# Kernel optimization log

Hardware: AMD Instinct MI355X
Metric: run time of the kernel (lower is better)

## Reference

```python
import jax, jax.numpy as jnp
import numpy as np

SAMPLE_RATE = 0.1
BINS = int(256 * SAMPLE_RATE)  # 25
KSIZE = 7
EPS = 1e-6


def _pascal_kernel_2d(ksize):
    # kornia get_pascal_kernel_2d(ksize, norm=True): outer product of binomial row, sum=1
    row = np.array([1.0, 6.0, 15.0, 20.0, 15.0, 6.0, 1.0], dtype=np.float32)
    row = row / row.sum()
    k2d = np.outer(row, row)
    return jnp.asarray(k2d, dtype=jnp.float32)


def _blur_pool2d(x, ksize=KSIZE):
    # kornia.filters.blur_pool2d: depthwise conv with pascal kernel, stride 2, zero pad ksize//2
    C = x.shape[1]
    k = jnp.broadcast_to(_pascal_kernel_2d(ksize).astype(x.dtype), (C, 1, ksize, ksize))
    pad = ksize // 2
    return jax.lax.conv_general_dilated(
        x, k, window_strides=(2, 2), padding=((pad, pad), (pad, pad)),
        feature_group_count=C, dimension_numbers=("NCHW", "OIHW", "NCHW"))


def _per_channel_hist(x, bins):
    # torch.histc(v, bins, 0, 1) per (b, c) plane: values outside [0,1] ignored,
    # value == 1 falls in last bin. Fused via one flat scatter-add.
    B, C, H, W = x.shape
    v = x.reshape(B * C, H * W)
    idx = jnp.clip(jnp.floor(v * bins).astype(jnp.int32), 0, bins - 1)
    valid = ((v >= 0.0) & (v <= 1.0)).astype(x.dtype)
    flat_idx = (jnp.arange(B * C, dtype=jnp.int32)[:, None] * bins + idx).reshape(-1)
    hist = jnp.zeros(B * C * bins, dtype=x.dtype).at[flat_idx].add(valid.reshape(-1))
    return hist.reshape(B, C, bins)


def setup_inputs() -> dict:
    key = jax.random.key(0)
    kx, ky = jax.random.split(key)
    B, C, H, W = 32, 3, 512, 512
    x = jax.random.uniform(kx, (B, C, H, W), dtype=jnp.float32)
    y = jax.random.uniform(ky, (B, C, H, W), dtype=jnp.float32)
    return {"x": x, "y": y}


def reference(x, y):
    hw = x.shape[-2] * x.shape[-1]  # original H*W (as in source)
    xb = _blur_pool2d(x)
    yb = _blur_pool2d(y)
    xh = _per_channel_hist(xb, BINS) / hw  # [B, C, BINS]
    yh = _per_channel_hist(yb, BINS) / hw
    # nn.CosineSimilarity(dim=0, eps=1e-6) applied per (b, c) vector pair
    dot = jnp.sum(xh * yh, axis=-1)
    nx = jnp.maximum(jnp.linalg.norm(xh, axis=-1), EPS)
    ny = jnp.maximum(jnp.linalg.norm(yh, axis=-1), EPS)
    cos = dot / (nx * ny)  # [B, C]
    return jnp.mean(cos)
```

## Files before the change

kernel.cpp:

```cpp
#include <hip/hip_runtime.h>

#define BINS 25
#define H 512
#define W 512
#define OH 256
#define OW 256
#define NPLANES 96
#define TOX 32
#define TOY 16
#define NBX 8
#define NBY 16
#define NBLK (NBX*NBY)
#define TROWS 37
#define LDW 72
#define RP 72
#define VP 36
#define NPAIR 35

__global__ __launch_bounds__(256) void blur_hist(
        const float* __restrict__ x, const float* __restrict__ y,
        unsigned int* __restrict__ partial) {
    const int z = blockIdx.z;
    const float* src = (z < NPLANES) ? x + (size_t)z * H * W
                                     : y + (size_t)(z - NPLANES) * H * W;

    __shared__ __align__(16) float raw[TROWS * RP];
    __shared__ float ve[TOY * VP];
    __shared__ float vo[TOY * VP];
    __shared__ unsigned int sh[4 * 32];

    const int tid = threadIdx.x;
    const int base_x = 2 * (blockIdx.x * TOX) - 4;
    const int base_y = 2 * (blockIdx.y * TOY) - 3;

    if (tid < 128) sh[tid] = 0u;

    const bool xfull = (base_x >= 0) && (base_x + LDW <= W);
    for (int v = tid; v < TROWS * (LDW / 4); v += 256) {
        int r  = v / (LDW / 4);
        int c4 = v - r * (LDW / 4);
        int gy = base_y + r;
        int gx = base_x + 4 * c4;
        float4 val = make_float4(0.f, 0.f, 0.f, 0.f);
        if (gy >= 0 && gy < H) {
            if (xfull) {
                val = *(const float4*)(src + (size_t)gy * W + gx);
            } else {
                const size_t rb = (size_t)gy * W;
                if (gx + 0 >= 0 && gx + 0 < W) val.x = src[rb + gx + 0];
                if (gx + 1 >= 0 && gx + 1 < W) val.y = src[rb + gx + 1];
                if (gx + 2 >= 0 && gx + 2 < W) val.z = src[rb + gx + 2];
                if (gx + 3 >= 0 && gx + 3 < W) val.w = src[rb + gx + 3];
            }
        }
        *(float4*)(raw + r * RP + 4 * c4) = val;
    }
    __syncthreads();

    const float w0 = 1.f/64.f, w1 = 6.f/64.f, w2 = 15.f/64.f, w3 = 20.f/64.f;

    for (int v = tid; v < TOY * NPAIR; v += 256) {
        int ly = v / NPAIR;
        int pr = v - ly * NPAIR;
        const float2* p = (const float2*)(raw + 2 * ly * RP + 2 * pr);
        float2 a0 = p[0 * (RP/2)], a1 = p[1 * (RP/2)], a2 = p[2 * (RP/2)],
               a3 = p[3 * (RP/2)], a4 = p[4 * (RP/2)], a5 = p[5 * (RP/2)],
               a6 = p[6 * (RP/2)];
        ve[ly * VP + pr] = w0*(a0.x+a6.x) + w1*(a1.x+a5.x) + w2*(a2.x+a4.x) + w3*a3.x;
        vo[ly * VP + pr] = w0*(a0.y+a6.y) + w1*(a1.y+a5.y) + w2*(a2.y+a4.y) + w3*a3.y;
    }
    __syncthreads();

    const int lx = tid & 31;
    unsigned int* wh = &sh[(tid >> 6) * 32];
    #pragma unroll
    for (int i = 0; i < 2; i++) {
        int ly = (tid >> 5) + 8 * i;
        const float* e = ve + ly * VP + lx;
        const float* o = vo + ly * VP + lx;
        float s = w0*(o[0] + o[3]) + w2*(o[1] + o[2]) + w1*(e[1] + e[3]) + w3*e[2];
        int b = min((int)(s * 25.f), BINS - 1);
        atomicAdd(&wh[b], 1u);
    }
    __syncthreads();

    if (tid < BINS) {
        unsigned int t = sh[tid] + sh[32 + tid] + sh[64 + tid] + sh[96 + tid];
        int blk = blockIdx.y * NBX + blockIdx.x;
        partial[((size_t)z * NBLK + blk) * BINS + tid] = t;
    }
}

__global__ __launch_bounds__(256) void reduce_cos(
        const unsigned int* __restrict__ partial, float* __restrict__ out) {
    __shared__ unsigned int sh[2 * BINS];
    const int p = blockIdx.x;
    const int t = threadIdx.x;
    if (t < 2 * BINS) sh[t] = 0u;
    __syncthreads();
    const unsigned int* xp = partial + (size_t)p * NBLK * BINS;
    const unsigned int* yp = partial + (size_t)(NPLANES + p) * NBLK * BINS;
    for (int f = t; f < NBLK * BINS; f += 256) {
        int b = f % BINS;
        atomicAdd(&sh[b], xp[f]);
        atomicAdd(&sh[BINS + b], yp[f]);
    }
    __syncthreads();
    if (t == 0) {
        const float inv_hw = 1.0f / (float)(H * W);
        float dot = 0.f, nx = 0.f, ny = 0.f;
        for (int i = 0; i < BINS; i++) {
            float a = (float)sh[i] * inv_hw;
            float b = (float)sh[BINS + i] * inv_hw;
            dot += a * b;
            nx  += a * a;
            ny  += b * b;
        }
        nx = fmaxf(sqrtf(nx), 1e-6f);
        ny = fmaxf(sqrtf(ny), 1e-6f);
        atomicAdd(out, (dot / (nx * ny)) * (1.0f / (float)NPLANES));
    }
}

extern "C" void kernel_launch(void* const* d_in, const int* in_sizes, int n_in,
                              void* d_out, int out_size, void* d_ws, size_t ws_size,
                              hipStream_t stream) {
    const float* x = (const float*)d_in[0];
    const float* y = (const float*)d_in[1];
    float* out = (float*)d_out;

    unsigned int* partial = (unsigned int*)d_ws;

    hipMemsetAsync(out, 0, sizeof(float), stream);

    dim3 grd(NBX, NBY, 2 * NPLANES);
    blur_hist<<<grd, 256, 0, stream>>>(x, y, partial);

    reduce_cos<<<NPLANES, 256, 0, stream>>>(partial, out);
}
```

Baseline: 232.2 us.

## Use async global-to-LDS loads for interior tiles and lane-private histograms

```diff
diff --git a/kernel.cpp b/kernel.cpp
--- a/kernel.cpp
+++ b/kernel.cpp
@@ -3,8 +3,6 @@
 #define BINS 25
 #define H 512
 #define W 512
-#define OH 256
-#define OW 256
 #define NPLANES 96
 #define TOX 32
 #define TOY 16
@@ -12,10 +10,17 @@
 #define NBY 16
 #define NBLK (NBX*NBY)
 #define TROWS 37
-#define LDW 72
 #define RP 72
+#define NV4 (TROWS*18)
 #define VP 36
-#define NPAIR 35
+#define NSH 32
+
+__device__ __forceinline__ void async_load16(const float* g, float* lds_wave_base) {
+    __builtin_amdgcn_global_load_lds(
+        (const __attribute__((address_space(1))) void*)g,
+        (__attribute__((address_space(3))) void*)lds_wave_base,
+        16, 0, 0);
+}
 
 __global__ __launch_bounds__(256) void blur_hist(
         const float* __restrict__ x, const float* __restrict__ y,
@@ -27,52 +32,68 @@
     __shared__ __align__(16) float raw[TROWS * RP];
     __shared__ float ve[TOY * VP];
     __shared__ float vo[TOY * VP];
-    __shared__ unsigned int sh[4 * 32];
+    __shared__ unsigned int sh[NSH * BINS];
 
     const int tid = threadIdx.x;
     const int base_x = 2 * (blockIdx.x * TOX) - 4;
     const int base_y = 2 * (blockIdx.y * TOY) - 3;
 
-    if (tid < 128) sh[tid] = 0u;
+    for (int i = tid; i < NSH * BINS; i += 256) sh[i] = 0u;
 
-    const bool xfull = (base_x >= 0) && (base_x + LDW <= W);
-    for (int v = tid; v < TROWS * (LDW / 4); v += 256) {
-        int r  = v / (LDW / 4);
-        int c4 = v - r * (LDW / 4);
-        int gy = base_y + r;
-        int gx = base_x + 4 * c4;
-        float4 val = make_float4(0.f, 0.f, 0.f, 0.f);
-        if (gy >= 0 && gy < H) {
-            if (xfull) {
-                val = *(const float4*)(src + (size_t)gy * W + gx);
-            } else {
-                const size_t rb = (size_t)gy * W;
-                if (gx + 0 >= 0 && gx + 0 < W) val.x = src[rb + gx + 0];
-                if (gx + 1 >= 0 && gx + 1 < W) val.y = src[rb + gx + 1];
-                if (gx + 2 >= 0 && gx + 2 < W) val.z = src[rb + gx + 2];
-                if (gx + 3 >= 0 && gx + 3 < W) val.w = src[rb + gx + 3];
+    const bool interior = (base_x >= 0) && (base_x + RP <= W) &&
+                          (base_y >= 0) && (base_y + TROWS <= H);
+    if (interior) {
+        #pragma unroll
+        for (int k = 0; k < 3; k++) {
+            int v = 256 * k + tid;
+            if (v < NV4) {
+                int r = v / 18;
+                int c = v - r * 18;
+                const float* g = src + (size_t)(base_y + r) * W + base_x + 4 * c;
+                float* dst = raw + (size_t)(256 * k + (tid & ~63)) * 4;
+                async_load16(g, dst);
             }
         }
-        *(float4*)(raw + r * RP + 4 * c4) = val;
+    } else {
+        const bool xfull = (base_x >= 0) && (base_x + RP <= W);
+        for (int v = tid; v < NV4; v += 256) {
+            int r  = v / 18;
+            int c4 = v - r * 18;
+            int gy = base_y + r;
+            int gx = base_x + 4 * c4;
+            float4 val = make_float4(0.f, 0.f, 0.f, 0.f);
+            if (gy >= 0 && gy < H) {
+                if (xfull) {
+                    val = *(const float4*)(src + (size_t)gy * W + gx);
+                } else {
+                    const size_t rb = (size_t)gy * W;
+                    if (gx + 0 >= 0 && gx + 0 < W) val.x = src[rb + gx + 0];
+                    if (gx + 1 >= 0 && gx + 1 < W) val.y = src[rb + gx + 1];
+                    if (gx + 2 >= 0 && gx + 2 < W) val.z = src[rb + gx + 2];
+                    if (gx + 3 >= 0 && gx + 3 < W) val.w = src[rb + gx + 3];
+                }
+            }
+            *(float4*)(raw + r * RP + 4 * c4) = val;
+        }
     }
     __syncthreads();
 
     const float w0 = 1.f/64.f, w1 = 6.f/64.f, w2 = 15.f/64.f, w3 = 20.f/64.f;
 
-    for (int v = tid; v < TOY * NPAIR; v += 256) {
-        int ly = v / NPAIR;
-        int pr = v - ly * NPAIR;
-        const float2* p = (const float2*)(raw + 2 * ly * RP + 2 * pr);
-        float2 a0 = p[0 * (RP/2)], a1 = p[1 * (RP/2)], a2 = p[2 * (RP/2)],
-               a3 = p[3 * (RP/2)], a4 = p[4 * (RP/2)], a5 = p[5 * (RP/2)],
-               a6 = p[6 * (RP/2)];
-        ve[ly * VP + pr] = w0*(a0.x+a6.x) + w1*(a1.x+a5.x) + w2*(a2.x+a4.x) + w3*a3.x;
-        vo[ly * VP + pr] = w0*(a0.y+a6.y) + w1*(a1.y+a5.y) + w2*(a2.y+a4.y) + w3*a3.y;
+    for (int v = tid; v < TOY * 70; v += 256) {
+        int ly = v / 70;
+        int t  = v - ly * 70;
+        const float* p = raw + (2 * ly) * RP + t;
+        float s = w0 * (p[0] + p[6 * RP]) + w1 * (p[1 * RP] + p[5 * RP])
+                + w2 * (p[2 * RP] + p[4 * RP]) + w3 * p[3 * RP];
+        int pr = t >> 1;
+        if (t & 1) vo[ly * VP + pr] = s;
+        else       ve[ly * VP + pr] = s;
     }
     __syncthreads();
 
     const int lx = tid & 31;
-    unsigned int* wh = &sh[(tid >> 6) * 32];
+    unsigned int* wh = sh + (tid & 31) * BINS;
     #pragma unroll
     for (int i = 0; i < 2; i++) {
         int ly = (tid >> 5) + 8 * i;
@@ -85,9 +106,11 @@
     __syncthreads();
 
     if (tid < BINS) {
-        unsigned int t = sh[tid] + sh[32 + tid] + sh[64 + tid] + sh[96 + tid];
+        unsigned int s = 0;
+        #pragma unroll
+        for (int g = 0; g < NSH; g++) s += sh[g * BINS + tid];
         int blk = blockIdx.y * NBX + blockIdx.x;
-        partial[((size_t)z * NBLK + blk) * BINS + tid] = t;
+        partial[((size_t)z * NBLK + blk) * BINS + tid] = s;
     }
 }
 
```

Measured after the change: 231.6 us. About the same (-0.3%).

## Replace shared-memory tiled blur with register sliding-window column strips

Applied to the files above, without the earlier changes.

```diff
diff --git a/kernel.cpp b/kernel.cpp
--- a/kernel.cpp
+++ b/kernel.cpp
@@ -3,118 +3,114 @@
 #define BINS 25
 #define H 512
 #define W 512
-#define OH 256
-#define OW 256
 #define NPLANES 96
-#define TOX 32
-#define TOY 16
-#define NBX 8
-#define NBY 16
-#define NBLK (NBX*NBY)
-#define TROWS 37
-#define LDW 72
-#define RP 72
-#define VP 36
-#define NPAIR 35
+#define NSH 32
 
 __global__ __launch_bounds__(256) void blur_hist(
         const float* __restrict__ x, const float* __restrict__ y,
         unsigned int* __restrict__ partial) {
-    const int z = blockIdx.z;
+    const int b = blockIdx.x;
+    const int z = b >> 2;
     const float* src = (z < NPLANES) ? x + (size_t)z * H * W
                                      : y + (size_t)(z - NPLANES) * H * W;
 
-    __shared__ __align__(16) float raw[TROWS * RP];
-    __shared__ float ve[TOY * VP];
-    __shared__ float vo[TOY * VP];
-    __shared__ unsigned int sh[4 * 32];
+    __shared__ unsigned int sh[NSH * BINS];
+    const int tid = threadIdx.x;
+    if (tid < (NSH * BINS / 4))
+        *(float4*)((float*)sh + 4 * tid) = make_float4(0.f, 0.f, 0.f, 0.f);
+    __syncthreads();
 
-    const int tid = threadIdx.x;
-    const int base_x = 2 * (blockIdx.x * TOX) - 4;
-    const int base_y = 2 * (blockIdx.y * TOY) - 3;
-
-    if (tid < 128) sh[tid] = 0u;
-
-    const bool xfull = (base_x >= 0) && (base_x + LDW <= W);
-    for (int v = tid; v < TROWS * (LDW / 4); v += 256) {
-        int r  = v / (LDW / 4);
-        int c4 = v - r * (LDW / 4);
-        int gy = base_y + r;
-        int gx = base_x + 4 * c4;
-        float4 val = make_float4(0.f, 0.f, 0.f, 0.f);
-        if (gy >= 0 && gy < H) {
-            if (xfull) {
-                val = *(const float4*)(src + (size_t)gy * W + gx);
-            } else {
-                const size_t rb = (size_t)gy * W;
-                if (gx + 0 >= 0 && gx + 0 < W) val.x = src[rb + gx + 0];
-                if (gx + 1 >= 0 && gx + 1 < W) val.y = src[rb + gx + 1];
-                if (gx + 2 >= 0 && gx + 2 < W) val.z = src[rb + gx + 2];
-                if (gx + 3 >= 0 && gx + 3 < W) val.w = src[rb + gx + 3];
-            }
-        }
-        *(float4*)(raw + r * RP + 4 * c4) = val;
-    }
-    __syncthreads();
+    const int i = tid & 63;
+    const int s = (b & 3) * 4 + (tid >> 6);
+    const int c0 = 8 * i - 4;
+    const int o0 = (i == 0)  ? 0   : c0;
+    const int o3 = (i == 63) ? 508 : c0 + 12;
+    const float m0 = (i == 0)  ? 0.f : 1.f;
+    const float m3 = (i == 63) ? 0.f : 1.f;
 
     const float w0 = 1.f/64.f, w1 = 6.f/64.f, w2 = 15.f/64.f, w3 = 20.f/64.f;
 
-    for (int v = tid; v < TOY * NPAIR; v += 256) {
-        int ly = v / NPAIR;
-        int pr = v - ly * NPAIR;
-        const float2* p = (const float2*)(raw + 2 * ly * RP + 2 * pr);
-        float2 a0 = p[0 * (RP/2)], a1 = p[1 * (RP/2)], a2 = p[2 * (RP/2)],
-               a3 = p[3 * (RP/2)], a4 = p[4 * (RP/2)], a5 = p[5 * (RP/2)],
-               a6 = p[6 * (RP/2)];
-        ve[ly * VP + pr] = w0*(a0.x+a6.x) + w1*(a1.x+a5.x) + w2*(a2.x+a4.x) + w3*a3.x;
-        vo[ly * VP + pr] = w0*(a0.y+a6.y) + w1*(a1.y+a5.y) + w2*(a2.y+a4.y) + w3*a3.y;
+    auto load_row = [&](int gy) -> float4 {
+        float4 h = make_float4(0.f, 0.f, 0.f, 0.f);
+        if ((unsigned)gy < (unsigned)H) {
+            const float* rp = src + (size_t)gy * W;
+            float4 Q0 = *(const float4*)(rp + o0);
+            float4 Q1 = *(const float4*)(rp + c0 + 4);
+            float4 Q2 = *(const float4*)(rp + c0 + 8);
+            float4 Q3 = *(const float4*)(rp + o3);
+            float r1 = Q0.y * m0, r2 = Q0.z * m0, r3 = Q0.w * m0;
+            float r4 = Q1.x, r5 = Q1.y, r6 = Q1.z, r7 = Q1.w;
+            float r8 = Q2.x, r9 = Q2.y, r10 = Q2.z, r11 = Q2.w;
+            float r12 = Q3.x * m3, r13 = Q3.y * m3;
+            h.x = w0*(r1 + r7)  + w1*(r2 + r6)  + w2*(r3 + r5)  + w3*r4;
+            h.y = w0*(r3 + r9)  + w1*(r4 + r8)  + w2*(r5 + r7)  + w3*r6;
+            h.z = w0*(r5 + r11) + w1*(r6 + r10) + w2*(r7 + r9)  + w3*r8;
+            h.w = w0*(r7 + r13) + w1*(r8 + r12) + w2*(r9 + r11) + w3*r10;
+        }
+        return h;
+    };
+
+    unsigned int* wh = sh + (tid & (NSH - 1)) * BINS;
+    auto binit = [&](float v) {
+        int bb = min((int)(v * 25.f), BINS - 1);
+        atomicAdd(&wh[bb], 1u);
+    };
+    auto vout = [&](const float4& h0, const float4& h1, const float4& h2,
+                    const float4& h3, const float4& h4, const float4& h5,
+                    const float4& h6) {
+        binit(w0*(h0.x+h6.x) + w1*(h1.x+h5.x) + w2*(h2.x+h4.x) + w3*h3.x);
+        binit(w0*(h0.y+h6.y) + w1*(h1.y+h5.y) + w2*(h2.y+h4.y) + w3*h3.y);
+        binit(w0*(h0.z+h6.z) + w1*(h1.z+h5.z) + w2*(h2.z+h4.z) + w3*h3.z);
+        binit(w0*(h0.w+h6.w) + w1*(h1.w+h5.w) + w2*(h2.w+h4.w) + w3*h3.w);
+    };
+
+    const int gy0 = 32 * s - 3;
+    float4 h0 = load_row(gy0 + 0), h1 = load_row(gy0 + 1), h2 = load_row(gy0 + 2),
+           h3 = load_row(gy0 + 3), h4 = load_row(gy0 + 4), h5 = load_row(gy0 + 5),
+           h6 = load_row(gy0 + 6);
+    #pragma unroll 5
+    for (int j = 0; j < 15; j++) {
+        float4 hA = load_row(gy0 + 7 + 2 * j);
+        float4 hB = load_row(gy0 + 8 + 2 * j);
+        vout(h0, h1, h2, h3, h4, h5, h6);
+        h0 = h2; h1 = h3; h2 = h4; h3 = h5; h4 = h6; h5 = hA; h6 = hB;
     }
-    __syncthreads();
-
-    const int lx = tid & 31;
-    unsigned int* wh = &sh[(tid >> 6) * 32];
-    #pragma unroll
-    for (int i = 0; i < 2; i++) {
-        int ly = (tid >> 5) + 8 * i;
-        const float* e = ve + ly * VP + lx;
-        const float* o = vo + ly * VP + lx;
-        float s = w0*(o[0] + o[3]) + w2*(o[1] + o[2]) + w1*(e[1] + e[3]) + w3*e[2];
-        int b = min((int)(s * 25.f), BINS - 1);
-        atomicAdd(&wh[b], 1u);
-    }
+    vout(h0, h1, h2, h3, h4, h5, h6);
     __syncthreads();
 
     if (tid < BINS) {
-        unsigned int t = sh[tid] + sh[32 + tid] + sh[64 + tid] + sh[96 + tid];
-        int blk = blockIdx.y * NBX + blockIdx.x;
-        partial[((size_t)z * NBLK + blk) * BINS + tid] = t;
+        unsigned int acc = 0;
+        #pragma unroll
+        for (int g = 0; g < NSH; g++) acc += sh[g * BINS + tid];
+        partial[b * BINS + tid] = acc;
     }
 }
 
-__global__ __launch_bounds__(256) void reduce_cos(
+__global__ __launch_bounds__(64) void reduce_cos(
         const unsigned int* __restrict__ partial, float* __restrict__ out) {
-    __shared__ unsigned int sh[2 * BINS];
+    __shared__ float sa[BINS], sb[BINS];
     const int p = blockIdx.x;
     const int t = threadIdx.x;
-    if (t < 2 * BINS) sh[t] = 0u;
-    __syncthreads();
-    const unsigned int* xp = partial + (size_t)p * NBLK * BINS;
-    const unsigned int* yp = partial + (size_t)(NPLANES + p) * NBLK * BINS;
-    for (int f = t; f < NBLK * BINS; f += 256) {
-        int b = f % BINS;
-        atomicAdd(&sh[b], xp[f]);
-        atomicAdd(&sh[BINS + b], yp[f]);
+    if (t < BINS) {
+        unsigned int a = 0, bb = 0;
+        #pragma unroll
+        for (int j = 0; j < 4; j++) {
+            a  += partial[((size_t)p * 4 + j) * BINS + t];
+            bb += partial[((size_t)(NPLANES + p) * 4 + j) * BINS + t];
+        }
+        sa[t] = (float)a;
+        sb[t] = (float)bb;
     }
     __syncthreads();
     if (t == 0) {
         const float inv_hw = 1.0f / (float)(H * W);
         float dot = 0.f, nx = 0.f, ny = 0.f;
-        for (int i = 0; i < BINS; i++) {
-            float a = (float)sh[i] * inv_hw;
-            float b = (float)sh[BINS + i] * inv_hw;
-            dot += a * b;
+        for (int k = 0; k < BINS; k++) {
+            float a = sa[k] * inv_hw;
+            float c = sb[k] * inv_hw;
+            dot += a * c;
             nx  += a * a;
-            ny  += b * b;
+            ny  += c * c;
         }
         nx = fmaxf(sqrtf(nx), 1e-6f);
         ny = fmaxf(sqrtf(ny), 1e-6f);
@@ -133,8 +129,6 @@
 
     hipMemsetAsync(out, 0, sizeof(float), stream);
 
-    dim3 grd(NBX, NBY, 2 * NPLANES);
-    blur_hist<<<grd, 256, 0, stream>>>(x, y, partial);
-
-    reduce_cos<<<NPLANES, 256, 0, stream>>>(partial, out);
+    blur_hist<<<768, 256, 0, stream>>>(x, y, partial);
+    reduce_cos<<<NPLANES, 64, 0, stream>>>(partial, out);
 }
```

New measurement: 219.4 us. -5.5%, faster.
